# Optimization experiments

Measured on AMD Instinct MI355X. Metric: run time of the kernel, lower is better.

Reference implementation:

```python
import jax, jax.numpy as jnp
import numpy as np

T, N, U, K, P = 4096, 256, 128, 32, 128


def setup_inputs() -> dict:
    key = jax.random.key(0)
    ks = jax.random.split(key, 8)
    input_sequence = jax.random.normal(ks[0], (T, U, K), jnp.float32)
    # Stable diagonal dynamics: |A| in (0.5, 0.99), random phase.
    r = jax.random.uniform(ks[1], (N, K), jnp.float32, 0.5, 0.99)
    theta = jax.random.uniform(ks[2], (N, K), jnp.float32, 0.0, np.pi)
    A_re = r * jnp.cos(theta)
    A_im = r * jnp.sin(theta)
    s_b = 1.0 / np.sqrt(U)
    s_c = 1.0 / np.sqrt(N)
    B_re = jax.random.normal(ks[3], (N, U), jnp.float32) * s_b
    B_im = jax.random.normal(ks[4], (N, U), jnp.float32) * s_b
    C_re = jax.random.normal(ks[5], (P, N), jnp.float32) * s_c
    C_im = jax.random.normal(ks[6], (P, N), jnp.float32) * s_c
    D = jax.random.normal(ks[7], (P, U), jnp.float32) * s_b
    return dict(input_sequence=input_sequence, A_re=A_re, A_im=A_im,
                B_re=B_re, B_im=B_im, C_re=C_re, C_im=C_im, D=D)


def _binary_op(elem_i, elem_j):
    # (a_i, s_i) o (a_j, s_j) = (a_i * a_j, a_j * s_i + s_j)
    a_i, s_i = elem_i
    a_j, s_j = elem_j
    return (a_i * a_j, a_j * s_i + s_j)


def reference(input_sequence, A_re, A_im, B_re, B_im, C_re, C_im, D):
    A = (A_re + 1j * A_im).astype(jnp.complex64)        # (N, K) diagonal
    Bm = (B_re + 1j * B_im).astype(jnp.complex64)        # (N, U)
    Cm = (C_re + 1j * C_im).astype(jnp.complex64)        # (P, N)
    x_c = input_sequence.astype(jnp.complex64)           # (T, U, K)
    # inputs_t = B @ x_t  -> (T, N, K)
    inputs = jnp.einsum('nu,tuk->tnk', Bm, x_c)
    systems = jnp.broadcast_to(A, (input_sequence.shape[0],) + A.shape)
    _, states = jax.lax.associative_scan(_binary_op, (systems, inputs))
    # out_t = C @ state_t -> (T, P, K)
    out = jnp.real(jnp.einsum('pn,tnk->tpk', Cm, states))
    Du = jnp.einsum('pu,tuk->tpk', D, input_sequence)    # 2D D branch
    return out + Du
```

## Files before the change

kernel.cpp:

```cpp
#include <hip/hip_runtime.h>
#include <hip/hip_bf16.h>

namespace {

constexpr int T = 4096, N = 256, U = 128, K = 32, P = 128;
constexpr int NK = N * K;
constexpr int CL = 64;
constexpr int NCH = T / CL;
constexpr int TB = 8;

typedef __attribute__((ext_vector_type(8))) short short8;
typedef __attribute__((ext_vector_type(4))) float f32x4;
typedef __attribute__((address_space(3))) unsigned lds_u32;
typedef __attribute__((address_space(1))) const unsigned glb_u32;

__device__ __forceinline__ unsigned short f2bf(float f) {
  union { float f; unsigned u; } v; v.f = f;
  unsigned r = v.u + 0x7FFFu + ((v.u >> 16) & 1u);
  return (unsigned short)(r >> 16);
}
__device__ __forceinline__ float bf2f(unsigned short s) {
  union { unsigned u; float f; } v; v.u = ((unsigned)s) << 16;
  return v.f;
}
__device__ __forceinline__ short8 ld8(const unsigned short* p) {
  return *reinterpret_cast<const short8*>(p);
}
__device__ __forceinline__ void dma16(const unsigned* g, unsigned* l) {
  __builtin_amdgcn_global_load_lds((glb_u32*)g, (lds_u32*)l, 16, 0, 0);
}

__device__ __forceinline__ int zswz(int k, int n) {
  int n8 = n >> 3, j = n & 7;
  return k * 256 + ((n8 ^ (k & 7)) << 3) + (j ^ (((k >> 3) & 1) << 2));
}

__device__ __forceinline__ void unpackAB(uint4 a, uint4 b, short8& re, short8& im) {
  union { short8 v; unsigned u[4]; } r, i;
  r.u[0] = (a.x & 0xFFFFu) | (a.y << 16);
  i.u[0] = (a.x >> 16)     | (a.y & 0xFFFF0000u);
  r.u[1] = (a.z & 0xFFFFu) | (a.w << 16);
  i.u[1] = (a.z >> 16)     | (a.w & 0xFFFF0000u);
  r.u[2] = (b.x & 0xFFFFu) | (b.y << 16);
  i.u[2] = (b.x >> 16)     | (b.y & 0xFFFF0000u);
  r.u[3] = (b.z & 0xFFFFu) | (b.w << 16);
  i.u[3] = (b.z >> 16)     | (b.w & 0xFFFF0000u);
  re = r.v; im = i.v;
}

__global__ __launch_bounds__(256) void k_params(
    const float* Are, const float* Aim, const float* Bre, const float* Bim,
    const float* Cre, const float* Cim, const float* D,
    unsigned short* bre, unsigned short* bim, unsigned short* cre,
    unsigned short* cimn, unsigned short* dbf, float* atre, float* atim) {
  int idx = blockIdx.x * 256 + threadIdx.x;
  int stride = gridDim.x * 256;
  for (int i = idx; i < N * U; i += stride) { bre[i] = f2bf(Bre[i]); bim[i] = f2bf(Bim[i]); }
  for (int i = idx; i < P * N; i += stride) { cre[i] = f2bf(Cre[i]); cimn[i] = f2bf(-Cim[i]); }
  for (int i = idx; i < P * U; i += stride) { dbf[i] = f2bf(D[i]); }
  for (int i = idx; i < NK; i += stride) {
    int k = i >> 8, r = i & 255;
    int n8 = (r >> 3) ^ (k & 7);
    int j  = (r & 7) ^ (((k >> 3) & 1) << 2);
    int n = n8 * 8 + j;
    atre[i] = Are[n * K + k];
    atim[i] = Aim[n * K + k];
  }
}

__global__ __launch_bounds__(256) void k_castx(const float* x, unsigned* xTu) {
  __shared__ float lds[U * 33];
  int t = blockIdx.x, tid = threadIdx.x;
  const float* xt = x + (size_t)t * (U * K);
#pragma unroll
  for (int it = 0; it < 16; it++) {
    int idx = it * 256 + tid;
    int u = idx >> 5, k = idx & 31;
    lds[u * 33 + k] = xt[idx];
  }
  __syncthreads();
  unsigned* dst = xTu + (size_t)t * (K * U / 2);
#pragma unroll
  for (int it = 0; it < 8; it++) {
    int k = it * 4 + (tid >> 6);
    int up = tid & 63;
    float f0 = lds[(2 * up) * 33 + k];
    float f1 = lds[(2 * up + 1) * 33 + k];
    dst[k * 64 + up] = (unsigned)f2bf(f0) | ((unsigned)f2bf(f1) << 16);
  }
}

__global__ __launch_bounds__(256)
__attribute__((amdgpu_waves_per_eu(2, 2)))
void k_bgemm(const unsigned short* xT, const unsigned short* bre,
             const unsigned short* bim, unsigned* zbuf, int t0) {
  int blk = blockIdx.x, tid = threadIdx.x;
  int w = tid >> 6, l = tid & 63, lq = l >> 4, lr = l & 15;
  short8 Bf_re[4][4], Bf_im[4][4];
#pragma unroll
  for (int s = 0; s < 4; s++)
#pragma unroll
    for (int nt = 0; nt < 4; nt++) {
      int n0 = (w * 4 + nt) * 16;
      Bf_re[s][nt] = ld8(bre + (n0 + lr) * U + s * 32 + lq * 8);
      Bf_im[s][nt] = ld8(bim + (n0 + lr) * U + s * 32 + lq * 8);
    }
#pragma unroll
  for (int tl = 0; tl < TB; tl++) {
    int tloc = blk * TB + tl;
    const unsigned short* xrow = xT + (size_t)(t0 + tloc) * (K * U);
    short8 af[4][2];
#pragma unroll
    for (int s = 0; s < 4; s++) {
      af[s][0] = ld8(xrow + lr * U + s * 32 + lq * 8);
      af[s][1] = ld8(xrow + (16 + lr) * U + s * 32 + lq * 8);
    }
    f32x4 accre[2][4], accim[2][4];
#pragma unroll
    for (int a = 0; a < 2; a++)
#pragma unroll
      for (int b = 0; b < 4; b++) { accre[a][b] = (f32x4)0.f; accim[a][b] = (f32x4)0.f; }
#pragma unroll
    for (int s = 0; s < 4; s++)
#pragma unroll
      for (int nt = 0; nt < 4; nt++)
#pragma unroll
        for (int mt = 0; mt < 2; mt++) {
          accre[mt][nt] = __builtin_amdgcn_mfma_f32_16x16x32_bf16(af[s][mt], Bf_re[s][nt], accre[mt][nt], 0, 0, 0);
          accim[mt][nt] = __builtin_amdgcn_mfma_f32_16x16x32_bf16(af[s][mt], Bf_im[s][nt], accim[mt][nt], 0, 0, 0);
        }
    unsigned* dst = zbuf + (size_t)tloc * NK;
#pragma unroll
    for (int mt = 0; mt < 2; mt++)
#pragma unroll
      for (int nt = 0; nt < 4; nt++) {
        int n0 = (w * 4 + nt) * 16;
#pragma unroll
        for (int r = 0; r < 4; r++) {
          int krow = mt * 16 + lq * 4 + r;
          dst[zswz(krow, n0 + lr)] =
              (unsigned)f2bf(accre[mt][nt][r]) | ((unsigned)f2bf(accim[mt][nt][r]) << 16);
        }
      }
  }
}

__global__ __launch_bounds__(256) void k_scanA(const unsigned* zbuf, const float* atre,
                                               const float* atim, float2* cend, int c0) {
  int bid = blockIdx.x;
  int cl = bid >> 5;
  int lane = (bid & 31) * 256 + threadIdx.x;
  float ar = atre[lane], ai = atim[lane];
  float sr = 0.f, si = 0.f;
  const unsigned* src = zbuf + (size_t)cl * CL * NK + lane;
#pragma unroll 8
  for (int i = 0; i < CL; i++) {
    unsigned v = src[(size_t)i * NK];
    float ur = bf2f((unsigned short)(v & 0xFFFFu));
    float ui = bf2f((unsigned short)(v >> 16));
    float nr = ar * sr - ai * si + ur;
    float ni = ar * si + ai * sr + ui;
    sr = nr; si = ni;
  }
  cend[(size_t)(c0 + cl) * NK + lane] = make_float2(sr, si);
}

__global__ __launch_bounds__(256) void k_scanB(float2* cend, const float* atre,
                                               const float* atim) {
  int lane = blockIdx.x * 256 + threadIdx.x;
  float pr = atre[lane], pi = atim[lane];
#pragma unroll
  for (int i = 0; i < 6; i++) { float nr = pr * pr - pi * pi, ni = 2.f * pr * pi; pr = nr; pi = ni; }
  float cr = 0.f, ci = 0.f;
  for (int g = 0; g < NCH / 8; g++) {
    float2 buf[8];
#pragma unroll
    for (int j = 0; j < 8; j++) buf[j] = cend[(size_t)(g * 8 + j) * NK + lane];
#pragma unroll
    for (int j = 0; j < 8; j++) {
      cend[(size_t)(g * 8 + j) * NK + lane] = make_float2(cr, ci);
      float nr = pr * cr - pi * ci + buf[j].x;
      float ni = pr * ci + pi * cr + buf[j].y;
      cr = nr; ci = ni;
    }
  }
}

__global__ __launch_bounds__(256) void k_scanC(unsigned* zbuf, const float* atre,
                                               const float* atim, const float2* cend, int c0) {
  int bid = blockIdx.x;
  int cl = bid >> 5;
  int lane = (bid & 31) * 256 + threadIdx.x;
  float ar = atre[lane], ai = atim[lane];
  float2 cin = cend[(size_t)(c0 + cl) * NK + lane];
  float sr = cin.x, si = cin.y;
  unsigned* p = zbuf + (size_t)cl * CL * NK + lane;
#pragma unroll 8
  for (int i = 0; i < CL; i++) {
    unsigned v = p[(size_t)i * NK];
    float ur = bf2f((unsigned short)(v & 0xFFFFu));
    float ui = bf2f((unsigned short)(v >> 16));
    float nr = ar * sr - ai * si + ur;
    float ni = ar * si + ai * sr + ui;
    sr = nr; si = ni;
    p[(size_t)i * NK] = (unsigned)f2bf(sr) | ((unsigned)f2bf(si) << 16);
  }
}

__global__ __launch_bounds__(256)
__attribute__((amdgpu_waves_per_eu(2, 2)))
void k_out(const unsigned* zbuf,
           const unsigned short* cre, const unsigned short* cimn,
           const unsigned short* dbf, const unsigned short* xT,
           float* out, int t0) {
  __shared__ unsigned ldsz[2][NK];
  int blk = blockIdx.x, tid = threadIdx.x;
  int w = tid >> 6, l = tid & 63, lq = l >> 4, lr = l & 15;
  int h = (lr >> 3) & 1;
  short8 Cf_re[8][2], Cf_im[8][2];
#pragma unroll
  for (int s = 0; s < 8; s++)
#pragma unroll
    for (int i = 0; i < 2; i++) {
      int p = (w * 2 + i) * 16 + lr;
      Cf_re[s][i] = ld8(cre  + p * N + s * 32 + lq * 8);
      Cf_im[s][i] = ld8(cimn + p * N + s * 32 + lq * 8);
    }
  short8 Df[4][2];
#pragma unroll
  for (int s = 0; s < 4; s++)
#pragma unroll
    for (int i = 0; i < 2; i++) {
      int p = (w * 2 + i) * 16 + lr;
      Df[s][i] = ld8(dbf + p * U + s * 32 + lq * 8);
    }
  {
    const unsigned* z0 = zbuf + (size_t)(blk * TB) * NK;
#pragma unroll
    for (int it = 0; it < 8; it++)
      dma16(z0 + it * 1024 + tid * 4, &ldsz[0][it * 1024 + tid * 4]);
  }
  __syncthreads();
  int cur = 0;
  for (int tl = 0; tl < TB; tl++) {
    int tloc = blk * TB + tl;
    int t = t0 + tloc;
    if (tl + 1 < TB) {
      const unsigned* zn = zbuf + (size_t)(tloc + 1) * NK;
#pragma unroll
      for (int it = 0; it < 8; it++)
        dma16(zn + it * 1024 + tid * 4, &ldsz[cur ^ 1][it * 1024 + tid * 4]);
    }
    const unsigned short* xt = xT + (size_t)t * (K * U);
    short8 xfr[4][2];
#pragma unroll
    for (int s = 0; s < 4; s++)
#pragma unroll
      for (int kt = 0; kt < 2; kt++)
        xfr[s][kt] = ld8(xt + (kt * 16 + lr) * U + s * 32 + lq * 8);
    f32x4 acc[2][2];
#pragma unroll
    for (int i = 0; i < 2; i++)
#pragma unroll
      for (int j = 0; j < 2; j++) acc[i][j] = (f32x4)0.f;
    const unsigned* zl = &ldsz[cur][0];
#pragma unroll
    for (int s = 0; s < 8; s++) {
      short8 bfr[2], bfi[2];
#pragma unroll
      for (int kt = 0; kt < 2; kt++) {
        int k = kt * 16 + lr;
        int n8 = s * 4 + lq;
        const uint4* q = reinterpret_cast<const uint4*>(zl + k * 256 + ((n8 ^ (k & 7)) << 3));
        uint4 a = q[h], b = q[h ^ 1];
        unpackAB(a, b, bfr[kt], bfi[kt]);
      }
#pragma unroll
      for (int i = 0; i < 2; i++)
#pragma unroll
        for (int kt = 0; kt < 2; kt++) {
          acc[i][kt] = __builtin_amdgcn_mfma_f32_16x16x32_bf16(Cf_re[s][i], bfr[kt], acc[i][kt], 0, 0, 0);
          acc[i][kt] = __builtin_amdgcn_mfma_f32_16x16x32_bf16(Cf_im[s][i], bfi[kt], acc[i][kt], 0, 0, 0);
        }
    }
#pragma unroll
    for (int s = 0; s < 4; s++)
#pragma unroll
      for (int i = 0; i < 2; i++)
#pragma unroll
        for (int kt = 0; kt < 2; kt++)
          acc[i][kt] = __builtin_amdgcn_mfma_f32_16x16x32_bf16(Df[s][i], xfr[s][kt], acc[i][kt], 0, 0, 0);
    float* ot = out + (size_t)t * (P * K);
#pragma unroll
    for (int i = 0; i < 2; i++)
#pragma unroll
      for (int kt = 0; kt < 2; kt++)
#pragma unroll
        for (int r = 0; r < 4; r++) {
          int p = (w * 2 + i) * 16 + lq * 4 + r;
          int k = kt * 16 + lr;
          ot[p * K + k] = acc[i][kt][r];
        }
    __syncthreads();
    cur ^= 1;
  }
}

}

extern "C" void kernel_launch(void* const* d_in, const int* in_sizes, int n_in,
                              void* d_out, int out_size, void* d_ws, size_t ws_size,
                              hipStream_t stream) {
  const float* x   = (const float*)d_in[0];
  const float* Are = (const float*)d_in[1];
  const float* Aim = (const float*)d_in[2];
  const float* Bre = (const float*)d_in[3];
  const float* Bim = (const float*)d_in[4];
  const float* Cre = (const float*)d_in[5];
  const float* Cim = (const float*)d_in[6];
  const float* D   = (const float*)d_in[7];
  float* out = (float*)d_out;

  auto al = [](size_t x_) { return (x_ + 255) & ~(size_t)255; };
  const size_t fixed = al((size_t)T * K * U * 2)
                     + al((size_t)NCH * NK * 8)
                     + 2 * al((size_t)N * U * 2)
                     + 2 * al((size_t)P * N * 2)
                     + al((size_t)P * U * 2)
                     + 2 * al((size_t)NK * 4);
  int S = 64;
  for (int s : {1, 2, 4, 8, 16, 32, 64}) {
    if (fixed + al((size_t)(T / s) * NK * 4) <= ws_size) { S = s; break; }
  }
  const int TS = T / S;
  const int CS = NCH / S;

  char* w = (char*)d_ws;
  auto alloc = [&](size_t bytes) { void* p = (void*)w; w += (bytes + 255) & ~(size_t)255; return p; };
  unsigned* zbuf       = (unsigned*)alloc((size_t)TS * NK * 4);
  unsigned* xTu        = (unsigned*)alloc((size_t)T * K * U * 2);
  float2* cend         = (float2*)alloc((size_t)NCH * NK * 8);
  unsigned short* bre  = (unsigned short*)alloc((size_t)N * U * 2);
  unsigned short* bim  = (unsigned short*)alloc((size_t)N * U * 2);
  unsigned short* cre  = (unsigned short*)alloc((size_t)P * N * 2);
  unsigned short* cimn = (unsigned short*)alloc((size_t)P * N * 2);
  unsigned short* dbf  = (unsigned short*)alloc((size_t)P * U * 2);
  float* atre          = (float*)alloc((size_t)NK * 4);
  float* atim          = (float*)alloc((size_t)NK * 4);

  k_params<<<64, 256, 0, stream>>>(Are, Aim, Bre, Bim, Cre, Cim, D,
                                   bre, bim, cre, cimn, dbf, atre, atim);
  k_castx<<<T, 256, 0, stream>>>(x, xTu);

  const unsigned short* xT16 = (const unsigned short*)xTu;
  for (int q = 0; q < S; q++) {
    k_bgemm<<<TS / TB, 256, 0, stream>>>(xT16, bre, bim, zbuf, q * TS);
    k_scanA<<<CS * 32, 256, 0, stream>>>(zbuf, atre, atim, cend, q * CS);
  }
  k_scanB<<<NK / 256, 256, 0, stream>>>(cend, atre, atim);
  for (int q = 0; q < S; q++) {
    if (S > 1)
      k_bgemm<<<TS / TB, 256, 0, stream>>>(xT16, bre, bim, zbuf, q * TS);
    k_scanC<<<CS * 32, 256, 0, stream>>>(zbuf, atre, atim, cend, q * CS);
    k_out<<<TS / TB, 256, 0, stream>>>(zbuf, cre, cimn, dbf, xT16, out, q * TS);
  }
}
```

Before: 311.1 us.

## Fuse chunk-local scan into output GEMM kernel and add hierarchical carry pass

Shrinks the scan chunk from 64 to 16 steps and replaces the single serial carry kernel with a three-level pass: group aggregate, serial group carry, then per-chunk carry fan-out. The separate scanC pass is dropped. Each block of the new 512-thread output kernel now walks its 16 timesteps in order, applying the recurrence to the LDS-staged z tile before running the MFMA output GEMM. This removes a full read-modify-write of the state buffer through global memory and shortens the serial carry chain. In exchange each block carries 64 float registers of scan state, adds an extra barrier per timestep, and launches more, smaller carry kernels.

```diff
diff --git a/kernel.cpp b/kernel.cpp
--- a/kernel.cpp
+++ b/kernel.cpp
@@ -5,8 +5,9 @@
 
 constexpr int T = 4096, N = 256, U = 128, K = 32, P = 128;
 constexpr int NK = N * K;
-constexpr int CL = 64;
+constexpr int CL = 16;
 constexpr int NCH = T / CL;
+constexpr int NG = NCH / 8;
 constexpr int TB = 8;
 
 typedef __attribute__((ext_vector_type(8))) short short8;
@@ -28,6 +29,9 @@
 }
 __device__ __forceinline__ void dma16(const unsigned* g, unsigned* l) {
   __builtin_amdgcn_global_load_lds((glb_u32*)g, (lds_u32*)l, 16, 0, 0);
+}
+__device__ __forceinline__ void csq(float& pr, float& pi) {
+  float nr = pr * pr - pi * pi, ni = 2.f * pr * pi; pr = nr; pi = ni;
 }
 
 __device__ __forceinline__ int zswz(int k, int n) {
@@ -165,20 +169,39 @@
   cend[(size_t)(c0 + cl) * NK + lane] = make_float2(sr, si);
 }
 
-__global__ __launch_bounds__(256) void k_scanB(float2* cend, const float* atre,
-                                               const float* atim) {
+__global__ __launch_bounds__(256) void k_carryg(const float2* cend, const float* atre,
+                                                const float* atim, float2* gagg) {
+  int bid = blockIdx.x;
+  int g = bid >> 5;
+  int lane = (bid & 31) * 256 + threadIdx.x;
+  float pr = atre[lane], pi = atim[lane];
+#pragma unroll
+  for (int i = 0; i < 4; i++) csq(pr, pi);
+  float agr = 0.f, agi = 0.f;
+#pragma unroll
+  for (int j = 0; j < 8; j++) {
+    float2 e = cend[(size_t)(g * 8 + j) * NK + lane];
+    float nr = pr * agr - pi * agi + e.x;
+    float ni = pr * agi + pi * agr + e.y;
+    agr = nr; agi = ni;
+  }
+  gagg[(size_t)g * NK + lane] = make_float2(agr, agi);
+}
+
+__global__ __launch_bounds__(256) void k_carryb(float2* gagg, const float* atre,
+                                                const float* atim) {
   int lane = blockIdx.x * 256 + threadIdx.x;
   float pr = atre[lane], pi = atim[lane];
 #pragma unroll
-  for (int i = 0; i < 6; i++) { float nr = pr * pr - pi * pi, ni = 2.f * pr * pi; pr = nr; pi = ni; }
+  for (int i = 0; i < 7; i++) csq(pr, pi);
   float cr = 0.f, ci = 0.f;
-  for (int g = 0; g < NCH / 8; g++) {
+  for (int gg = 0; gg < NG / 8; gg++) {
     float2 buf[8];
 #pragma unroll
-    for (int j = 0; j < 8; j++) buf[j] = cend[(size_t)(g * 8 + j) * NK + lane];
+    for (int j = 0; j < 8; j++) buf[j] = gagg[(size_t)(gg * 8 + j) * NK + lane];
 #pragma unroll
     for (int j = 0; j < 8; j++) {
-      cend[(size_t)(g * 8 + j) * NK + lane] = make_float2(cr, ci);
+      gagg[(size_t)(gg * 8 + j) * NK + lane] = make_float2(cr, ci);
       float nr = pr * cr - pi * ci + buf[j].x;
       float ni = pr * ci + pi * cr + buf[j].y;
       cr = nr; ci = ni;
@@ -186,70 +209,79 @@
   }
 }
 
-__global__ __launch_bounds__(256) void k_scanC(unsigned* zbuf, const float* atre,
-                                               const float* atim, const float2* cend, int c0) {
+__global__ __launch_bounds__(256) void k_carryf(float2* cend, const float* atre,
+                                                const float* atim, const float2* gagg) {
   int bid = blockIdx.x;
-  int cl = bid >> 5;
+  int g = bid >> 5;
   int lane = (bid & 31) * 256 + threadIdx.x;
-  float ar = atre[lane], ai = atim[lane];
-  float2 cin = cend[(size_t)(c0 + cl) * NK + lane];
-  float sr = cin.x, si = cin.y;
-  unsigned* p = zbuf + (size_t)cl * CL * NK + lane;
-#pragma unroll 8
-  for (int i = 0; i < CL; i++) {
-    unsigned v = p[(size_t)i * NK];
-    float ur = bf2f((unsigned short)(v & 0xFFFFu));
-    float ui = bf2f((unsigned short)(v >> 16));
-    float nr = ar * sr - ai * si + ur;
-    float ni = ar * si + ai * sr + ui;
-    sr = nr; si = ni;
-    p[(size_t)i * NK] = (unsigned)f2bf(sr) | ((unsigned)f2bf(si) << 16);
-  }
-}
-
-__global__ __launch_bounds__(256)
+  float pr = atre[lane], pi = atim[lane];
+#pragma unroll
+  for (int i = 0; i < 4; i++) csq(pr, pi);
+  float2 c = gagg[(size_t)g * NK + lane];
+  float cr = c.x, ci = c.y;
+#pragma unroll
+  for (int j = 0; j < 8; j++) {
+    size_t off = (size_t)(g * 8 + j) * NK + lane;
+    float2 e = cend[off];
+    cend[off] = make_float2(cr, ci);
+    float nr = pr * cr - pi * ci + e.x;
+    float ni = pr * ci + pi * cr + e.y;
+    cr = nr; ci = ni;
+  }
+}
+
+__global__ __launch_bounds__(512)
 __attribute__((amdgpu_waves_per_eu(2, 2)))
-void k_out(const unsigned* zbuf,
-           const unsigned short* cre, const unsigned short* cimn,
-           const unsigned short* dbf, const unsigned short* xT,
-           float* out, int t0) {
+void k_scout(const unsigned* zbuf, const float* atre, const float* atim,
+             const float2* cend,
+             const unsigned short* cre, const unsigned short* cimn,
+             const unsigned short* dbf, const unsigned short* xT,
+             float* out, int t0, int gc0) {
   __shared__ unsigned ldsz[2][NK];
   int blk = blockIdx.x, tid = threadIdx.x;
   int w = tid >> 6, l = tid & 63, lq = l >> 4, lr = l & 15;
   int h = (lr >> 3) & 1;
-  short8 Cf_re[8][2], Cf_im[8][2];
-#pragma unroll
-  for (int s = 0; s < 8; s++)
-#pragma unroll
-    for (int i = 0; i < 2; i++) {
-      int p = (w * 2 + i) * 16 + lr;
-      Cf_re[s][i] = ld8(cre  + p * N + s * 32 + lq * 8);
-      Cf_im[s][i] = ld8(cimn + p * N + s * 32 + lq * 8);
-    }
-  short8 Df[4][2];
-#pragma unroll
-  for (int s = 0; s < 4; s++)
-#pragma unroll
-    for (int i = 0; i < 2; i++) {
-      int p = (w * 2 + i) * 16 + lr;
-      Df[s][i] = ld8(dbf + p * U + s * 32 + lq * 8);
+  short8 Cf_re[8], Cf_im[8];
+#pragma unroll
+  for (int s = 0; s < 8; s++) {
+    int p = w * 16 + lr;
+    Cf_re[s] = ld8(cre  + p * N + s * 32 + lq * 8);
+    Cf_im[s] = ld8(cimn + p * N + s * 32 + lq * 8);
+  }
+  short8 Df[4];
+#pragma unroll
+  for (int s = 0; s < 4; s++) {
+    int p = w * 16 + lr;
+    Df[s] = ld8(dbf + p * U + s * 32 + lq * 8);
+  }
+  float ar[16], ai[16], sr[16], si[16];
+  int gc = gc0 + blk;
+#pragma unroll
+  for (int it = 0; it < 4; it++)
+#pragma unroll
+    for (int j = 0; j < 4; j++) {
+      int idx = it * 2048 + tid * 4 + j;
+      int e = it * 4 + j;
+      ar[e] = atre[idx]; ai[e] = atim[idx];
+      float2 c0 = cend[(size_t)gc * NK + idx];
+      sr[e] = c0.x; si[e] = c0.y;
     }
   {
-    const unsigned* z0 = zbuf + (size_t)(blk * TB) * NK;
-#pragma unroll
-    for (int it = 0; it < 8; it++)
-      dma16(z0 + it * 1024 + tid * 4, &ldsz[0][it * 1024 + tid * 4]);
+    const unsigned* z0 = zbuf + (size_t)(blk * CL) * NK;
+#pragma unroll
+    for (int it = 0; it < 4; it++)
+      dma16(z0 + it * 2048 + tid * 4, &ldsz[0][it * 2048 + tid * 4]);
   }
   __syncthreads();
   int cur = 0;
-  for (int tl = 0; tl < TB; tl++) {
-    int tloc = blk * TB + tl;
+  for (int tl = 0; tl < CL; tl++) {
+    int tloc = blk * CL + tl;
     int t = t0 + tloc;
-    if (tl + 1 < TB) {
+    if (tl + 1 < CL) {
       const unsigned* zn = zbuf + (size_t)(tloc + 1) * NK;
 #pragma unroll
-      for (int it = 0; it < 8; it++)
-        dma16(zn + it * 1024 + tid * 4, &ldsz[cur ^ 1][it * 1024 + tid * 4]);
+      for (int it = 0; it < 4; it++)
+        dma16(zn + it * 2048 + tid * 4, &ldsz[cur ^ 1][it * 2048 + tid * 4]);
     }
     const unsigned short* xt = xT + (size_t)t * (K * U);
     short8 xfr[4][2];
@@ -258,12 +290,31 @@
 #pragma unroll
       for (int kt = 0; kt < 2; kt++)
         xfr[s][kt] = ld8(xt + (kt * 16 + lr) * U + s * 32 + lq * 8);
-    f32x4 acc[2][2];
-#pragma unroll
-    for (int i = 0; i < 2; i++)
-#pragma unroll
-      for (int j = 0; j < 2; j++) acc[i][j] = (f32x4)0.f;
-    const unsigned* zl = &ldsz[cur][0];
+    unsigned* zl = &ldsz[cur][0];
+#pragma unroll
+    for (int it = 0; it < 4; it++) {
+      unsigned* p4 = zl + it * 2048 + tid * 4;
+      uint4 v = *reinterpret_cast<const uint4*>(p4);
+      unsigned d0 = v.x, d1 = v.y, d2 = v.z, d3 = v.w;
+#pragma unroll
+      for (int j = 0; j < 4; j++) {
+        unsigned dv = (j == 0) ? d0 : (j == 1) ? d1 : (j == 2) ? d2 : d3;
+        int e = it * 4 + j;
+        float ur = bf2f((unsigned short)(dv & 0xFFFFu));
+        float ui = bf2f((unsigned short)(dv >> 16));
+        float nr = ar[e] * sr[e] - ai[e] * si[e] + ur;
+        float ni = ar[e] * si[e] + ai[e] * sr[e] + ui;
+        sr[e] = nr; si[e] = ni;
+        dv = (unsigned)f2bf(nr) | ((unsigned)f2bf(ni) << 16);
+        if (j == 0) d0 = dv; else if (j == 1) d1 = dv; else if (j == 2) d2 = dv; else d3 = dv;
+      }
+      uint4 o; o.x = d0; o.y = d1; o.z = d2; o.w = d3;
+      *reinterpret_cast<uint4*>(p4) = o;
+    }
+    __syncthreads();
+    f32x4 acc[2];
+    acc[0] = (f32x4)0.f; acc[1] = (f32x4)0.f;
+    const unsigned* zs = &ldsz[cur][0];
 #pragma unroll
     for (int s = 0; s < 8; s++) {
       short8 bfr[2], bfi[2];
@@ -271,36 +322,30 @@
       for (int kt = 0; kt < 2; kt++) {
         int k = kt * 16 + lr;
         int n8 = s * 4 + lq;
-        const uint4* q = reinterpret_cast<const uint4*>(zl + k * 256 + ((n8 ^ (k & 7)) << 3));
-        uint4 a = q[h], b = q[h ^ 1];
+        const uint4* qp = reinterpret_cast<const uint4*>(zs + k * 256 + ((n8 ^ (k & 7)) << 3));
+        uint4 a = qp[h], b = qp[h ^ 1];
         unpackAB(a, b, bfr[kt], bfi[kt]);
       }
 #pragma unroll
-      for (int i = 0; i < 2; i++)
-#pragma unroll
-        for (int kt = 0; kt < 2; kt++) {
-          acc[i][kt] = __builtin_amdgcn_mfma_f32_16x16x32_bf16(Cf_re[s][i], bfr[kt], acc[i][kt], 0, 0, 0);
-          acc[i][kt] = __builtin_amdgcn_mfma_f32_16x16x32_bf16(Cf_im[s][i], bfi[kt], acc[i][kt], 0, 0, 0);
-        }
+      for (int kt = 0; kt < 2; kt++) {
+        acc[kt] = __builtin_amdgcn_mfma_f32_16x16x32_bf16(Cf_re[s], bfr[kt], acc[kt], 0, 0, 0);
+        acc[kt] = __builtin_amdgcn_mfma_f32_16x16x32_bf16(Cf_im[s], bfi[kt], acc[kt], 0, 0, 0);
+      }
     }
 #pragma unroll
     for (int s = 0; s < 4; s++)
 #pragma unroll
-      for (int i = 0; i < 2; i++)
-#pragma unroll
-        for (int kt = 0; kt < 2; kt++)
-          acc[i][kt] = __builtin_amdgcn_mfma_f32_16x16x32_bf16(Df[s][i], xfr[s][kt], acc[i][kt], 0, 0, 0);
+      for (int kt = 0; kt < 2; kt++)
+        acc[kt] = __builtin_amdgcn_mfma_f32_16x16x32_bf16(Df[s], xfr[s][kt], acc[kt], 0, 0, 0);
     float* ot = out + (size_t)t * (P * K);
 #pragma unroll
-    for (int i = 0; i < 2; i++)
-#pragma unroll
-      for (int kt = 0; kt < 2; kt++)
-#pragma unroll
-        for (int r = 0; r < 4; r++) {
-          int p = (w * 2 + i) * 16 + lq * 4 + r;
-          int k = kt * 16 + lr;
-          ot[p * K + k] = acc[i][kt][r];
-        }
+    for (int kt = 0; kt < 2; kt++)
+#pragma unroll
+      for (int r = 0; r < 4; r++) {
+        int p = w * 16 + lq * 4 + r;
+        int k = kt * 16 + lr;
+        ot[p * K + k] = acc[kt][r];
+      }
     __syncthreads();
     cur ^= 1;
   }
@@ -324,6 +369,7 @@
   auto al = [](size_t x_) { return (x_ + 255) & ~(size_t)255; };
   const size_t fixed = al((size_t)T * K * U * 2)
                      + al((size_t)NCH * NK * 8)
+                     + al((size_t)NG * NK * 8)
                      + 2 * al((size_t)N * U * 2)
                      + 2 * al((size_t)P * N * 2)
                      + al((size_t)P * U * 2)
@@ -340,6 +386,7 @@
   unsigned* zbuf       = (unsigned*)alloc((size_t)TS * NK * 4);
   unsigned* xTu        = (unsigned*)alloc((size_t)T * K * U * 2);
   float2* cend         = (float2*)alloc((size_t)NCH * NK * 8);
+  float2* gagg         = (float2*)alloc((size_t)NG * NK * 8);
   unsigned short* bre  = (unsigned short*)alloc((size_t)N * U * 2);
   unsigned short* bim  = (unsigned short*)alloc((size_t)N * U * 2);
   unsigned short* cre  = (unsigned short*)alloc((size_t)P * N * 2);
@@ -357,11 +404,13 @@
     k_bgemm<<<TS / TB, 256, 0, stream>>>(xT16, bre, bim, zbuf, q * TS);
     k_scanA<<<CS * 32, 256, 0, stream>>>(zbuf, atre, atim, cend, q * CS);
   }
-  k_scanB<<<NK / 256, 256, 0, stream>>>(cend, atre, atim);
+  k_carryg<<<NG * 32, 256, 0, stream>>>(cend, atre, atim, gagg);
+  k_carryb<<<NK / 256, 256, 0, stream>>>(gagg, atre, atim);
+  k_carryf<<<NG * 32, 256, 0, stream>>>(cend, atre, atim, gagg);
   for (int q = 0; q < S; q++) {
     if (S > 1)
       k_bgemm<<<TS / TB, 256, 0, stream>>>(xT16, bre, bim, zbuf, q * TS);
-    k_scanC<<<CS * 32, 256, 0, stream>>>(zbuf, atre, atim, cend, q * CS);
-    k_out<<<TS / TB, 256, 0, stream>>>(zbuf, cre, cimn, dbf, xT16, out, q * TS);
-  }
-}
+    k_scout<<<TS / CL, 512, 0, stream>>>(zbuf, atre, atim, cend,
+                                         cre, cimn, dbf, xT16, out, q * TS, q * CS);
+  }
+}
```

New measurement: 269.1 us. 13.5% less time.
